# Performance work log

Hardware: AMD Instinct MI355X
Metric: run time of the kernel (lower is better)

## Reference

```python
import jax, jax.numpy as jnp
import numpy as np

TEMPERATURE = 0.07
EPS = 1e-8  # F.cosine_similarity eps


def setup_inputs() -> dict:
    key = jax.random.key(0)
    k1, k2, k3, k4 = jax.random.split(key, 4)
    N, D, M, C = 4096, 1024, 8192, 100
    q = jax.random.normal(k1, (N, D), dtype=jnp.float32)
    labels = jax.random.randint(k2, (N,), 0, C, dtype=jnp.int32)
    memory_logits = jax.random.normal(k3, (N, M), dtype=jnp.float32)
    memory_targets = jax.random.bernoulli(k4, 0.5, (N, M)).astype(jnp.float32)
    return {"q": q, "labels": labels, "memory_logits": memory_logits,
            "memory_targets": memory_targets}


def reference(q, labels, memory_logits, memory_targets):
    N = q.shape[0]
    # cosine similarity as normalize + GEMM (second operand detached, as in torch)
    qn = q / jnp.maximum(jnp.linalg.norm(q, axis=-1, keepdims=True), EPS)
    sims = qn @ jax.lax.stop_gradient(qn).T               # [N, N]
    src_contrast = sims / TEMPERATURE
    logits_max = jax.lax.stop_gradient(
        jnp.max(src_contrast, axis=1, keepdims=True))
    src_logits = src_contrast - logits_max                # [N, N]
    # positive-pair mask with self excluded
    src_targets = (labels[:, None] == labels[None, :]).astype(jnp.float32)
    self_mask = 1.0 - jnp.eye(N, dtype=jnp.float32)
    src_targets = src_targets * self_mask
    targets = jnp.concatenate([src_targets, memory_targets], axis=1)  # [N, N+M]
    src_exp_logits = jnp.exp(src_logits) * self_mask
    logits = jnp.concatenate([src_logits, memory_logits], axis=1)     # [N, N+M]
    denom = src_exp_logits.sum(axis=1) + jnp.exp(memory_logits).sum(axis=1)
    log_prob = logits - jnp.log(denom)[:, None]
    mean_log_prob_pos = (targets * log_prob).sum(axis=1) / targets.sum(axis=1)
    return -jnp.mean(mean_log_prob_pos)
```

## Files before the change

### kernel.cpp

```cpp
#include <hip/hip_runtime.h>
#include <hip/hip_bf16.h>
#include <math.h>

typedef unsigned short u16;
typedef __bf16 bf16x8 __attribute__((ext_vector_type(8)));
typedef float f32x4 __attribute__((ext_vector_type(4)));
typedef unsigned short u16x4 __attribute__((ext_vector_type(4)));

#define NROW 4096
#define KDIM 1024
#define MDIM 8192
#define TILE 128
#define BK 64
#define NT   (NROW / TILE)
#define NSEG (NT * 2)
#define NTRI (NT * (NT + 1) / 2)

__device__ __forceinline__ u16 f2bf(float x) {
    unsigned int u = __float_as_uint(x);
    unsigned int r = (u + 0x7fffu + ((u >> 16) & 1u)) >> 16;
    return (u16)r;
}

__device__ __forceinline__ void gload16(const u16* g, u16* l) {
    __builtin_amdgcn_global_load_lds(
        (const __attribute__((address_space(1))) void*)g,
        (__attribute__((address_space(3))) void*)l,
        16, 0, 0);
}

__global__ void k_normalize(const float* __restrict__ q, u16* __restrict__ qn) {
    const int r = blockIdx.x;
    const int t = threadIdx.x;
    const int lane = t & 63, wid = t >> 6;
    const float4* qr = (const float4*)(q + (size_t)r * KDIM);
    float4 v = qr[t];
    float ss = v.x * v.x + v.y * v.y + v.z * v.z + v.w * v.w;
    #pragma unroll
    for (int d = 1; d < 64; d <<= 1) ss += __shfl_xor(ss, d);
    __shared__ float red[4];
    if (lane == 0) red[wid] = ss;
    __syncthreads();
    float tot = red[0] + red[1] + red[2] + red[3];
    float inv = 1.0f / fmaxf(sqrtf(tot), 1e-8f);
    u16x4 o;
    o[0] = f2bf(v.x * inv); o[1] = f2bf(v.y * inv);
    o[2] = f2bf(v.z * inv); o[3] = f2bf(v.w * inv);
    *(u16x4*)(qn + (size_t)r * KDIM + t * 4) = o;
}

__global__ void k_memstats(const float* __restrict__ ml, const float* __restrict__ mt,
                           float4* __restrict__ out) {
    const int r = blockIdx.x;
    const int t = threadIdx.x;
    const int lane = t & 63, wid = t >> 6;
    const float4* pl = (const float4*)(ml + (size_t)r * MDIM);
    const float4* pt = (const float4*)(mt + (size_t)r * MDIM);
    float S2 = 0.f, dot = 0.f, smt = 0.f;
    #pragma unroll
    for (int it = 0; it < 2; ++it) {
        const int i0 = it * 1024 + t;
        float4 l0 = pl[i0], l1 = pl[i0 + 256], l2 = pl[i0 + 512], l3 = pl[i0 + 768];
        float4 t0 = pt[i0], t1 = pt[i0 + 256], t2 = pt[i0 + 512], t3 = pt[i0 + 768];
        S2 += __expf(l0.x) + __expf(l0.y) + __expf(l0.z) + __expf(l0.w);
        S2 += __expf(l1.x) + __expf(l1.y) + __expf(l1.z) + __expf(l1.w);
        S2 += __expf(l2.x) + __expf(l2.y) + __expf(l2.z) + __expf(l2.w);
        S2 += __expf(l3.x) + __expf(l3.y) + __expf(l3.z) + __expf(l3.w);
        dot += t0.x * l0.x + t0.y * l0.y + t0.z * l0.z + t0.w * l0.w;
        dot += t1.x * l1.x + t1.y * l1.y + t1.z * l1.z + t1.w * l1.w;
        dot += t2.x * l2.x + t2.y * l2.y + t2.z * l2.z + t2.w * l2.w;
        dot += t3.x * l3.x + t3.y * l3.y + t3.z * l3.z + t3.w * l3.w;
        smt += t0.x + t0.y + t0.z + t0.w + t1.x + t1.y + t1.z + t1.w;
        smt += t2.x + t2.y + t2.z + t2.w + t3.x + t3.y + t3.z + t3.w;
    }
    #pragma unroll
    for (int d = 1; d < 64; d <<= 1) {
        S2  += __shfl_xor(S2, d);
        dot += __shfl_xor(dot, d);
        smt += __shfl_xor(smt, d);
    }
    __shared__ float red[4][3];
    if (lane == 0) { red[wid][0] = S2; red[wid][1] = dot; red[wid][2] = smt; }
    __syncthreads();
    if (t == 0)
        out[r] = make_float4(red[0][0] + red[1][0] + red[2][0] + red[3][0],
                             red[0][1] + red[1][1] + red[2][1] + red[3][1],
                             red[0][2] + red[1][2] + red[2][2] + red[3][2], 0.f);
}

__global__ void k_gemm_sym(const u16* __restrict__ qn, const int* __restrict__ labels,
                           float4* __restrict__ partials) {
    __shared__ u16 ldsA[TILE * BK];
    __shared__ u16 ldsB[TILE * BK];
    __shared__ int labR[TILE], labC[TILE];

    int u = blockIdx.x, bi = 0;
    while (u >= NT - bi) { u -= NT - bi; ++bi; }
    const int ct = bi + u;

    const int t = threadIdx.x;
    const int w = t >> 6, lane = t & 63;
    const int rowbase = bi * TILE, colbase = ct * TILE;

    if (t < 128) labR[t] = labels[rowbase + t];
    else labC[t - 128] = labels[colbase + (t - 128)];

    const int wr = (w >> 1) * 64, wc = (w & 1) * 64;
    const int cl = lane & 15, cg = lane >> 4;
    const int sr = lane >> 3, skb = lane & 7;

    f32x4 acc[4][4];
    #pragma unroll
    for (int i = 0; i < 4; ++i)
        #pragma unroll
        for (int j = 0; j < 4; ++j)
            acc[i][j] = {0.f, 0.f, 0.f, 0.f};

    for (int ks = 0; ks < KDIM / BK; ++ks) {
        const int k0 = ks * BK;
        #pragma unroll
        for (int it = 0; it < 4; ++it) {
            int c = w * 4 + it;
            int rr = c * 8 + sr;
            gload16(qn + (size_t)(rowbase + rr) * KDIM + k0 + skb * 8, ldsA + c * 512);
            gload16(qn + (size_t)(colbase + rr) * KDIM + k0 + skb * 8, ldsB + c * 512);
        }
        asm volatile("s_waitcnt vmcnt(0)" ::: "memory");
        __syncthreads();
        #pragma unroll
        for (int k2 = 0; k2 < 2; ++k2) {
            bf16x8 a[4], b[4];
            #pragma unroll
            for (int f = 0; f < 4; ++f) {
                a[f] = *(const bf16x8*)&ldsA[(wr + f * 16 + cl) * BK + k2 * 32 + cg * 8];
                b[f] = *(const bf16x8*)&ldsB[(wc + f * 16 + cl) * BK + k2 * 32 + cg * 8];
            }
            #pragma unroll
            for (int fm = 0; fm < 4; ++fm)
                #pragma unroll
                for (int fn = 0; fn < 4; ++fn)
                    acc[fm][fn] = __builtin_amdgcn_mfma_f32_16x16x32_bf16(
                        a[fm], b[fn], acc[fm][fn], 0, 0, 0);
        }
        __syncthreads();
    }

    const float invT = (float)(1.0 / 0.07);

    #pragma unroll
    for (int fm = 0; fm < 4; ++fm) {
        #pragma unroll
        for (int reg = 0; reg < 4; ++reg) {
            const int lr = wr + fm * 16 + cg * 4 + reg;
            const int gi = rowbase + lr;
            const int li = labR[lr];
            float c0 = acc[fm][0][reg] * invT;
            float c1 = acc[fm][1][reg] * invT;
            float c2 = acc[fm][2][reg] * invT;
            float c3 = acc[fm][3][reg] * invT;
            float m = fmaxf(fmaxf(c0, c1), fmaxf(c2, c3));
            #pragma unroll
            for (int d = 1; d < 16; d <<= 1) m = fmaxf(m, __shfl_xor(m, d));
            float se = 0.f, ps = 0.f, cnt = 0.f;
            #pragma unroll
            for (int fn = 0; fn < 4; ++fn) {
                float c = (fn == 0) ? c0 : (fn == 1) ? c1 : (fn == 2) ? c2 : c3;
                const int lc = wc + fn * 16 + cl;
                const bool self = (colbase + lc == gi);
                se += self ? 0.f : __expf(c - m);
                const bool pos = (!self) && (labC[lc] == li);
                ps += pos ? c : 0.f;
                cnt += pos ? 1.f : 0.f;
            }
            #pragma unroll
            for (int d = 1; d < 16; d <<= 1) {
                se  += __shfl_xor(se, d);
                ps  += __shfl_xor(ps, d);
                cnt += __shfl_xor(cnt, d);
            }
            if (cl == 0)
                partials[(size_t)(ct * 2 + (w & 1)) * NROW + gi] =
                    make_float4(m, se, ps, cnt);
        }
    }

    if (bi != ct) {
        #pragma unroll
        for (int fn = 0; fn < 4; ++fn) {
            const int lc = wc + fn * 16 + cl;
            const int gj = colbase + lc;
            const int lj = labC[lc];
            float m = -3.4e38f;
            #pragma unroll
            for (int fm = 0; fm < 4; ++fm)
                #pragma unroll
                for (int reg = 0; reg < 4; ++reg)
                    m = fmaxf(m, acc[fm][fn][reg] * invT);
            m = fmaxf(m, __shfl_xor(m, 16));
            m = fmaxf(m, __shfl_xor(m, 32));
            float se = 0.f, ps = 0.f, cnt = 0.f;
            #pragma unroll
            for (int fm = 0; fm < 4; ++fm) {
                #pragma unroll
                for (int reg = 0; reg < 4; ++reg) {
                    float c = acc[fm][fn][reg] * invT;
                    const int lr = wr + fm * 16 + cg * 4 + reg;
                    se += __expf(c - m);
                    const bool pos = (labR[lr] == lj);
                    ps += pos ? c : 0.f;
                    cnt += pos ? 1.f : 0.f;
                }
            }
            se += __shfl_xor(se, 16); ps += __shfl_xor(ps, 16); cnt += __shfl_xor(cnt, 16);
            se += __shfl_xor(se, 32); ps += __shfl_xor(ps, 32); cnt += __shfl_xor(cnt, 32);
            if (cg == 0)
                partials[(size_t)(bi * 2 + (w >> 1)) * NROW + gj] =
                    make_float4(m, se, ps, cnt);
        }
    }
}

__global__ void k_combine(const float4* __restrict__ partials, const float4* __restrict__ memq,
                          float* __restrict__ vals) {
    const int r = blockIdx.x * blockDim.x + threadIdx.x;
    if (r >= NROW) return;
    float M = -3.4e38f;
    #pragma unroll 8
    for (int s = 0; s < NSEG; ++s) M = fmaxf(M, partials[(size_t)s * NROW + r].x);
    float S1 = 0.f, ps = 0.f, cnt = 0.f;
    #pragma unroll 8
    for (int s = 0; s < NSEG; ++s) {
        float4 p = partials[(size_t)s * NROW + r];
        S1 += p.y * __expf(p.x - M);
        ps += p.z;
        cnt += p.w;
    }
    float4 mq = memq[r];
    float L = logf(S1 + mq.x);
    vals[r] = (ps - cnt * (M + L) + mq.y - mq.z * L) / (cnt + mq.z);
}

__global__ void k_finalize(const float* __restrict__ vals, float* __restrict__ out) {
    const int t = threadIdx.x;
    const int lane = t & 63, wid = t >> 6;
    float s = 0.f;
    for (int i = t; i < NROW; i += 256) s += vals[i];
    #pragma unroll
    for (int d = 1; d < 64; d <<= 1) s += __shfl_xor(s, d);
    __shared__ float red[4];
    if (lane == 0) red[wid] = s;
    __syncthreads();
    if (t == 0) out[0] = -(red[0] + red[1] + red[2] + red[3]) * (1.0f / (float)NROW);
}

extern "C" void kernel_launch(void* const* d_in, const int* in_sizes, int n_in,
                              void* d_out, int out_size, void* d_ws, size_t ws_size,
                              hipStream_t stream) {
    const float* q  = (const float*)d_in[0];
    const int* labels = (const int*)d_in[1];
    const float* ml = (const float*)d_in[2];
    const float* mt = (const float*)d_in[3];
    float* out = (float*)d_out;

    char* w = (char*)d_ws;
    u16* qn          = (u16*)w;
    float4* partials = (float4*)(w + 8388608);
    float4* memq     = (float4*)(w + 12582912);
    float* vals      = (float*)(w + 12648448);

    k_normalize<<<NROW, 256, 0, stream>>>(q, qn);
    k_memstats<<<NROW, 256, 0, stream>>>(ml, mt, memq);
    k_gemm_sym<<<NTRI, 256, 0, stream>>>(qn, labels, partials);
    k_combine<<<NROW / 256, 256, 0, stream>>>(partials, memq, vals);
    k_finalize<<<1, 256, 0, stream>>>(vals, out);
}
```

Measured before the change: 111.4 us.

## Fuse normalize with memory stats and remap GEMM tiles into XCD-local super-blocks

Merges the row-normalization kernel and the memory-bank statistics kernel into one launch, so both read their row in a single block and one launch plus its tail is removed. Also replaces the linear triangular tile index with a mapping that assigns each of 8 block-id residues (likely one per XCD) a contiguous set of 66 tiles drawn from 8x8 super-blocks of the upper triangle. The aim is better L2 reuse of qn rows and columns within each XCD. The mapping hard-codes NT=32 and NTRI=528.

```diff
diff --git a/kernel.cpp b/kernel.cpp
--- a/kernel.cpp
+++ b/kernel.cpp
@@ -29,31 +29,17 @@
         16, 0, 0);
 }
 
-__global__ void k_normalize(const float* __restrict__ q, u16* __restrict__ qn) {
+__global__ void k_norm_mem(const float* __restrict__ q,
+                           const float* __restrict__ ml, const float* __restrict__ mt,
+                           u16* __restrict__ qn, float4* __restrict__ memq) {
     const int r = blockIdx.x;
     const int t = threadIdx.x;
     const int lane = t & 63, wid = t >> 6;
+
     const float4* qr = (const float4*)(q + (size_t)r * KDIM);
     float4 v = qr[t];
     float ss = v.x * v.x + v.y * v.y + v.z * v.z + v.w * v.w;
-    #pragma unroll
-    for (int d = 1; d < 64; d <<= 1) ss += __shfl_xor(ss, d);
-    __shared__ float red[4];
-    if (lane == 0) red[wid] = ss;
-    __syncthreads();
-    float tot = red[0] + red[1] + red[2] + red[3];
-    float inv = 1.0f / fmaxf(sqrtf(tot), 1e-8f);
-    u16x4 o;
-    o[0] = f2bf(v.x * inv); o[1] = f2bf(v.y * inv);
-    o[2] = f2bf(v.z * inv); o[3] = f2bf(v.w * inv);
-    *(u16x4*)(qn + (size_t)r * KDIM + t * 4) = o;
-}
-
-__global__ void k_memstats(const float* __restrict__ ml, const float* __restrict__ mt,
-                           float4* __restrict__ out) {
-    const int r = blockIdx.x;
-    const int t = threadIdx.x;
-    const int lane = t & 63, wid = t >> 6;
+
     const float4* pl = (const float4*)(ml + (size_t)r * MDIM);
     const float4* pt = (const float4*)(mt + (size_t)r * MDIM);
     float S2 = 0.f, dot = 0.f, smt = 0.f;
@@ -73,6 +59,19 @@
         smt += t0.x + t0.y + t0.z + t0.w + t1.x + t1.y + t1.z + t1.w;
         smt += t2.x + t2.y + t2.z + t2.w + t3.x + t3.y + t3.z + t3.w;
     }
+
+    #pragma unroll
+    for (int d = 1; d < 64; d <<= 1) ss += __shfl_xor(ss, d);
+    __shared__ float redn[4];
+    if (lane == 0) redn[wid] = ss;
+    __syncthreads();
+    float tot = redn[0] + redn[1] + redn[2] + redn[3];
+    float inv = 1.0f / fmaxf(sqrtf(tot), 1e-8f);
+    u16x4 o;
+    o[0] = f2bf(v.x * inv); o[1] = f2bf(v.y * inv);
+    o[2] = f2bf(v.z * inv); o[3] = f2bf(v.w * inv);
+    *(u16x4*)(qn + (size_t)r * KDIM + t * 4) = o;
+
     #pragma unroll
     for (int d = 1; d < 64; d <<= 1) {
         S2  += __shfl_xor(S2, d);
@@ -83,9 +82,9 @@
     if (lane == 0) { red[wid][0] = S2; red[wid][1] = dot; red[wid][2] = smt; }
     __syncthreads();
     if (t == 0)
-        out[r] = make_float4(red[0][0] + red[1][0] + red[2][0] + red[3][0],
-                             red[0][1] + red[1][1] + red[2][1] + red[3][1],
-                             red[0][2] + red[1][2] + red[2][2] + red[3][2], 0.f);
+        memq[r] = make_float4(red[0][0] + red[1][0] + red[2][0] + red[3][0],
+                              red[0][1] + red[1][1] + red[2][1] + red[3][1],
+                              red[0][2] + red[1][2] + red[2][2] + red[3][2], 0.f);
 }
 
 __global__ void k_gemm_sym(const u16* __restrict__ qn, const int* __restrict__ labels,
@@ -94,9 +93,28 @@
     __shared__ u16 ldsB[TILE * BK];
     __shared__ int labR[TILE], labC[TILE];
 
-    int u = blockIdx.x, bi = 0;
-    while (u >= NT - bi) { u -= NT - bi; ++bi; }
-    const int ct = bi + u;
+    const int bid = blockIdx.x;
+    int e = (bid & 7) * 66 + (bid >> 3);
+    int rb, cb, base;
+    if      (e < 36)  { rb = 0; cb = 0; base = 0;   }
+    else if (e < 100) { rb = 0; cb = 1; base = 36;  }
+    else if (e < 136) { rb = 1; cb = 1; base = 100; }
+    else if (e < 200) { rb = 0; cb = 2; base = 136; }
+    else if (e < 264) { rb = 1; cb = 2; base = 200; }
+    else if (e < 300) { rb = 2; cb = 2; base = 264; }
+    else if (e < 364) { rb = 0; cb = 3; base = 300; }
+    else if (e < 428) { rb = 1; cb = 3; base = 364; }
+    else if (e < 492) { rb = 2; cb = 3; base = 428; }
+    else              { rb = 3; cb = 3; base = 492; }
+    int k = e - base;
+    int bi, ct;
+    if (rb == cb) {
+        int b2 = 0, kk = k;
+        while (kk >= 8 - b2) { kk -= 8 - b2; ++b2; }
+        bi = rb * 8 + b2; ct = cb * 8 + b2 + kk;
+    } else {
+        bi = rb * 8 + (k >> 3); ct = cb * 8 + (k & 7);
+    }
 
     const int t = threadIdx.x;
     const int w = t >> 6, lane = t & 63;
@@ -268,8 +286,7 @@
     float4* memq     = (float4*)(w + 12582912);
     float* vals      = (float*)(w + 12648448);
 
-    k_normalize<<<NROW, 256, 0, stream>>>(q, qn);
-    k_memstats<<<NROW, 256, 0, stream>>>(ml, mt, memq);
+    k_norm_mem<<<NROW, 256, 0, stream>>>(q, ml, mt, qn, memq);
     k_gemm_sym<<<NTRI, 256, 0, stream>>>(qn, labels, partials);
     k_combine<<<NROW / 256, 256, 0, stream>>>(partials, memq, vals);
     k_finalize<<<1, 256, 0, stream>>>(vals, out);
```

After: 108.7 us. -2.3%, faster.
